# Optimization experiments

Hardware: AMD Instinct MI355X
Metric: run time of the kernel (lower is better)

Reference implementation:

```python
import jax, jax.numpy as jnp
import numpy as np

N, F, H = 22, 448, 64
LN_EPS = 1e-5


def _layernorm(h, g, b):
    mu = h.mean(axis=-1, keepdims=True)
    var = ((h - mu) ** 2).mean(axis=-1, keepdims=True)
    return (h - mu) / jnp.sqrt(var + LN_EPS) * g + b


def setup_inputs() -> dict:
    key = jax.random.key(0)
    ks = jax.random.split(key, 16)
    B = 128
    x = jax.random.normal(ks[0], (B, N, F), dtype=jnp.float32)
    s = lambda fan_in: 1.0 / np.sqrt(fan_in)
    # correlation-branch edge_weight_net: Linear(2F,64) -> ReLU -> Linear(64,1) -> Sigmoid
    cw1 = jax.random.uniform(ks[1], (2 * F, 64), jnp.float32, -s(2 * F), s(2 * F))
    cb1 = jax.random.uniform(ks[2], (64,), jnp.float32, -s(2 * F), s(2 * F))
    cw2 = jax.random.uniform(ks[3], (64, 1), jnp.float32, -s(64), s(64))
    cb2 = jax.random.uniform(ks[4], (1,), jnp.float32, -s(64), s(64))
    # semantic branch
    emb = jax.random.normal(ks[5], (N, H), dtype=jnp.float32) * 0.01
    D = 2 * H + 2 * F
    sw1 = jax.random.uniform(ks[6], (D, H), jnp.float32, -s(D), s(D))
    sb1 = jax.random.uniform(ks[7], (H,), jnp.float32, -s(D), s(D))
    ln_g = jnp.ones((H,), jnp.float32)
    ln_b = jnp.zeros((H,), jnp.float32)
    sw2 = jax.random.uniform(ks[8], (H, H // 2), jnp.float32, -s(H), s(H))
    sb2 = jax.random.uniform(ks[9], (H // 2,), jnp.float32, -s(H), s(H))
    sw3 = jax.random.uniform(ks[10], (H // 2, 1), jnp.float32, -s(H // 2), s(H // 2))
    sb3 = jax.random.uniform(ks[11], (1,), jnp.float32, -s(H // 2), s(H // 2))
    thr = jnp.asarray(0.3, jnp.float32)
    alpha_p = jnp.asarray(0.6, jnp.float32)
    return dict(x=x, cw1=cw1, cb1=cb1, cw2=cw2, cb2=cb2, emb=emb,
                sw1=sw1, sb1=sb1, ln_g=ln_g, ln_b=ln_b,
                sw2=sw2, sb2=sb2, sw3=sw3, sb3=sb3,
                thr=thr, alpha_p=alpha_p)


def reference(x, cw1, cb1, cw2, cb2, emb, sw1, sb1, ln_g, ln_b,
              sw2, sb2, sw3, sb3, thr, alpha_p):
    B, n, f = x.shape
    eye = jnp.eye(n, dtype=x.dtype)[None]

    # ---- Correlation graph ----
    xc = x - x.mean(axis=-1, keepdims=True)
    std = jnp.std(x, axis=-1, ddof=1, keepdims=True) + 1e-8  # torch std is unbiased
    xn = xc / std
    corr = jnp.abs(jnp.einsum('bif,bjf->bij', xn, xn) / f)
    # pairwise edge features (B,N,N,2F)
    xi = jnp.broadcast_to(x[:, :, None, :], (B, n, n, f))
    xj = jnp.broadcast_to(x[:, None, :, :], (B, n, n, f))
    ef = jnp.concatenate([xi, xj], axis=-1)
    h = jax.nn.relu(ef @ cw1 + cb1)
    w_corr = jax.nn.sigmoid((h @ cw2 + cb2)[..., 0])
    g_corr = corr * w_corr + eye

    # ---- Semantic graph ----
    ei = jnp.broadcast_to(emb[None, :, None, :], (B, n, n, H))
    ej = jnp.broadcast_to(emb[None, None, :, :], (B, n, n, H))
    sf = jnp.concatenate([ei, ej, xi, xj], axis=-1)  # (B,N,N,2H+2F)
    h1 = jax.nn.relu(_layernorm(sf @ sw1 + sb1, ln_g, ln_b))
    h2 = jax.nn.relu(h1 @ sw2 + sb2)
    w_sem = jax.nn.sigmoid((h2 @ sw3 + sb3)[..., 0])  # (B,N,N)
    # original loop fills only i<j and mirrors; diagonal stays 0
    upper = jnp.triu(w_sem, k=1)
    adj = upper + jnp.swapaxes(upper, 1, 2)
    t = jax.nn.sigmoid(thr)
    adj = jnp.where(adj > t, adj, jnp.zeros_like(adj))
    g_sem = adj + eye

    # ---- Learned fusion ----
    alpha = jax.nn.sigmoid(alpha_p)
    return alpha * g_corr + (1.0 - alpha) * g_sem
```

## Files before the change

kernel.cpp:

```cpp
#include <hip/hip_runtime.h>
#include <math.h>

namespace {
constexpr int kN = 22;
constexpr int kF = 448;
constexpr int kNP = kN * kN;
constexpr int kXStr = 452;
constexpr int kSm1 = kN * kXStr + 2 * kN;
constexpr int kAStr = 36;
constexpr int kBStr = 68;
constexpr int kPStr = 68;
}

__global__ __launch_bounds__(256) void hgc_k1(
    const float* __restrict__ x,
    const float* __restrict__ cw1, const float* __restrict__ cb1,
    const float* __restrict__ emb,
    const float* __restrict__ sw1, const float* __restrict__ sb1,
    float* __restrict__ C, float* __restrict__ g,
    int M, int Mtiles, int nGemm)
{
    __shared__ __align__(16) float sm[kSm1];
    const int tid = threadIdx.x;

    if ((int)blockIdx.x < nGemm) {
        float* As = sm;
        float* Bs = sm + 64 * kAStr;
        const int bm = blockIdx.x % Mtiles;
        const int bn = blockIdx.x / Mtiles;
        const int m0 = bm * 32;

        const float* Wsrc =
            (bn == 0) ? cw1 :
            (bn == 1) ? cw1 + 448 * 64 :
            (bn == 2) ? sw1 + 128 * 64 :
                        sw1 + 576 * 64;

        const int tm = tid & 15;
        const int tn = tid >> 4;
        float acc[2][4];
        #pragma unroll
        for (int i = 0; i < 2; ++i)
            #pragma unroll
            for (int j = 0; j < 4; ++j) acc[i][j] = 0.f;

        for (int k0 = 0; k0 < kF; k0 += 64) {
            #pragma unroll
            for (int pass = 0; pass < 2; ++pass) {
                const int idx = tid + pass * 256;
                const int row = idx >> 4, kq = idx & 15;
                const int m = m0 + row;
                float4 v = {0, 0, 0, 0};
                if (m < M) v = *(const float4*)&x[(size_t)m * kF + k0 + kq * 4];
                As[(kq * 4 + 0) * kAStr + row] = v.x;
                As[(kq * 4 + 1) * kAStr + row] = v.y;
                As[(kq * 4 + 2) * kAStr + row] = v.z;
                As[(kq * 4 + 3) * kAStr + row] = v.w;
            }
            #pragma unroll
            for (int pass = 0; pass < 4; ++pass) {
                const int idx = tid + pass * 256;
                const int k = idx >> 4, nq = idx & 15;
                const float4 v = *(const float4*)&Wsrc[(size_t)(k0 + k) * 64 + nq * 4];
                *(float4*)&Bs[k * kBStr + nq * 4] = v;
            }
            __syncthreads();
            #pragma unroll 8
            for (int k = 0; k < 64; ++k) {
                const float2 a2 = *(const float2*)&As[k * kAStr + tm * 2];
                const float4 b4 = *(const float4*)&Bs[k * kBStr + tn * 4];
                acc[0][0] = fmaf(a2.x, b4.x, acc[0][0]);
                acc[0][1] = fmaf(a2.x, b4.y, acc[0][1]);
                acc[0][2] = fmaf(a2.x, b4.z, acc[0][2]);
                acc[0][3] = fmaf(a2.x, b4.w, acc[0][3]);
                acc[1][0] = fmaf(a2.y, b4.x, acc[1][0]);
                acc[1][1] = fmaf(a2.y, b4.y, acc[1][1]);
                acc[1][2] = fmaf(a2.y, b4.z, acc[1][2]);
                acc[1][3] = fmaf(a2.y, b4.w, acc[1][3]);
            }
            __syncthreads();
        }

        if (bn >= 2) {
            const float* W2 = sw1 + (bn == 2 ? 0 : 64) * 64;
            #pragma unroll
            for (int pass = 0; pass < 2; ++pass) {
                const int idx = tid + pass * 256;
                const int row = idx >> 4, kq = idx & 15;
                const int r = (m0 + row) % kN;
                const float4 v = *(const float4*)&emb[(size_t)r * 64 + kq * 4];
                As[(kq * 4 + 0) * kAStr + row] = v.x;
                As[(kq * 4 + 1) * kAStr + row] = v.y;
                As[(kq * 4 + 2) * kAStr + row] = v.z;
                As[(kq * 4 + 3) * kAStr + row] = v.w;
            }
            #pragma unroll
            for (int pass = 0; pass < 4; ++pass) {
                const int idx = tid + pass * 256;
                const int k = idx >> 4, nq = idx & 15;
                const float4 v = *(const float4*)&W2[(size_t)k * 64 + nq * 4];
                *(float4*)&Bs[k * kBStr + nq * 4] = v;
            }
            __syncthreads();
            #pragma unroll 8
            for (int k = 0; k < 64; ++k) {
                const float2 a2 = *(const float2*)&As[k * kAStr + tm * 2];
                const float4 b4 = *(const float4*)&Bs[k * kBStr + tn * 4];
                acc[0][0] = fmaf(a2.x, b4.x, acc[0][0]);
                acc[0][1] = fmaf(a2.x, b4.y, acc[0][1]);
                acc[0][2] = fmaf(a2.x, b4.z, acc[0][2]);
                acc[0][3] = fmaf(a2.x, b4.w, acc[0][3]);
                acc[1][0] = fmaf(a2.y, b4.x, acc[1][0]);
                acc[1][1] = fmaf(a2.y, b4.y, acc[1][1]);
                acc[1][2] = fmaf(a2.y, b4.z, acc[1][2]);
                acc[1][3] = fmaf(a2.y, b4.w, acc[1][3]);
            }
        }

        float4 bias = {0, 0, 0, 0};
        if (bn == 0)      bias = *(const float4*)&cb1[tn * 4];
        else if (bn == 2) bias = *(const float4*)&sb1[tn * 4];
        #pragma unroll
        for (int i = 0; i < 2; ++i) {
            const int m = m0 + tm * 2 + i;
            if (m < M) {
                float4 o;
                o.x = acc[i][0] + bias.x; o.y = acc[i][1] + bias.y;
                o.z = acc[i][2] + bias.z; o.w = acc[i][3] + bias.w;
                *(float4*)&C[(size_t)m * 256 + bn * 64 + tn * 4] = o;
            }
        }
    } else {
        float* smu = sm + kN * kXStr;
        float* sis = smu + kN;
        const int cb = blockIdx.x - nGemm;
        const int b = cb >> 1;
        const int r0 = (cb & 1) * 11;

        const float4* xb4 = (const float4*)(x + (size_t)b * (kN * kF));
        for (int idx = tid; idx < kN * kF / 4; idx += 256) {
            const float4 v = xb4[idx];
            const int r = idx / 112;
            const int k = (idx - r * 112) * 4;
            float* d = sm + r * kXStr + k;
            d[0] = v.x; d[1] = v.y; d[2] = v.z; d[3] = v.w;
        }
        __syncthreads();

        {
            const int wid = tid >> 6, lane = tid & 63;
            for (int r = wid; r < kN; r += 4) {
                const float* row = sm + r * kXStr;
                float s = 0.f;
                #pragma unroll
                for (int c = 0; c < 7; ++c) s += row[c * 64 + lane];
                #pragma unroll
                for (int o = 32; o; o >>= 1) s += __shfl_xor(s, o, 64);
                const float mean = s * (1.f / 448.f);
                float ss = 0.f;
                #pragma unroll
                for (int c = 0; c < 7; ++c) { const float d = row[c * 64 + lane] - mean; ss = fmaf(d, d, ss); }
                #pragma unroll
                for (int o = 32; o; o >>= 1) ss += __shfl_xor(ss, o, 64);
                if (lane == 0) {
                    smu[r] = mean;
                    sis[r] = 1.f / (sqrtf(ss * (1.f / 447.f)) + 1e-8f);
                }
            }
        }
        __syncthreads();

        for (int p = tid; p < 11 * kN; p += 256) {
            const int pi = p / 22;
            const int i = r0 + pi, j = p - pi * 22;
            const float4* ri = (const float4*)(sm + i * kXStr);
            const float4* rj = (const float4*)(sm + j * kXStr);
            float dot = 0.f;
            for (int q = 0; q < 112; ++q) {
                const float4 a = ri[q], bq = rj[q];
                dot = fmaf(a.x, bq.x, dot); dot = fmaf(a.y, bq.y, dot);
                dot = fmaf(a.z, bq.z, dot); dot = fmaf(a.w, bq.w, dot);
            }
            const float c = (dot - 448.f * smu[i] * smu[j]) * sis[i] * sis[j] * (1.f / 448.f);
            g[(size_t)b * kNP + i * 22 + j] = fabsf(c);
        }
    }
}

__global__ __launch_bounds__(256) void hgc_k2(
    const float* __restrict__ C, const float* __restrict__ g,
    const float* __restrict__ cw2, const float* __restrict__ cb2,
    const float* __restrict__ sw2, const float* __restrict__ sb2,
    const float* __restrict__ sw3, const float* __restrict__ sb3,
    const float* __restrict__ ln_g, const float* __restrict__ ln_b,
    const float* __restrict__ thr, const float* __restrict__ alpha_p,
    float* __restrict__ out)
{
    __shared__ __align__(16) float sp[4 * kN * kPStr];
    __shared__ float sg[kNP];
    __shared__ __align__(16) float sw2s[2048];
    __shared__ float scw2[64], slng[64], slnb[64], ssw3[32], ssb2[32];
    __shared__ float vbuf[32 * 66];

    const int tid = threadIdx.x;
    const int b   = blockIdx.x >> 2;
    const int pb  = blockIdx.x & 3;

    #pragma unroll
    for (int a = 0; a < 4; ++a) {
        float* dst = sp + a * kN * kPStr;
        for (int idx = tid; idx < 352; idx += 256) {
            const int r = idx >> 4, kq = idx & 15;
            const float4 v = *(const float4*)&C[((size_t)(b * 22 + r)) * 256 + a * 64 + kq * 4];
            *(float4*)&dst[r * kPStr + kq * 4] = v;
        }
    }
    for (int idx = tid; idx < kNP; idx += 256) sg[idx] = g[(size_t)b * kNP + idx];
    {
        const float4* s4 = (const float4*)sw2;
        for (int idx = tid; idx < 512; idx += 256)
            *((float4*)(sw2s + idx * 4)) = s4[idx];
    }
    if (tid < 64)       { scw2[tid] = cw2[tid]; slng[tid] = ln_g[tid]; slnb[tid] = ln_b[tid]; }
    else if (tid < 96)  { ssw3[tid - 64] = sw3[tid - 64]; }
    else if (tid < 128) { ssb2[tid - 96] = sb2[tid - 96]; }
    __syncthreads();

    const int pl = tid >> 3;
    const int t  = tid & 7;
    const float* sa1 = sp;
    const float* sa2 = sp + kN * kPStr;
    const float* su1 = sp + 2 * kN * kPStr;
    const float* su2 = sp + 3 * kN * kPStr;

    for (int ch = 0; ch < 4; ++ch) {
        const int lp = ch * 32 + pl;
        const bool valid = lp < 121;
        const int p = valid ? (pb * 121 + lp) : 0;
        const int i = p / 22, j = p - (p / 22) * 22;

        float zc = 0.f;
        {
            const float* pa1 = sa1 + i * kPStr + t * 8;
            const float* pa2 = sa2 + j * kPStr + t * 8;
            #pragma unroll
            for (int c = 0; c < 8; ++c) {
                const float h = fmaxf(pa1[c] + pa2[c], 0.f);
                zc = fmaf(h, scw2[t * 8 + c], zc);
            }
            zc += __shfl_xor(zc, 1, 64); zc += __shfl_xor(zc, 2, 64); zc += __shfl_xor(zc, 4, 64);
        }
        const float wc = 1.f / (1.f + __expf(-(zc + cb2[0])));

        const int lo = (i < j) ? i : j, hi = (i < j) ? j : i;
        const float* pu1 = su1 + lo * kPStr + t * 8;
        const float* pu2 = su2 + hi * kPStr + t * 8;
        float raw[8];
        float s1 = 0.f;
        #pragma unroll
        for (int c = 0; c < 8; ++c) { raw[c] = pu1[c] + pu2[c]; s1 += raw[c]; }
        s1 += __shfl_xor(s1, 1, 64); s1 += __shfl_xor(s1, 2, 64); s1 += __shfl_xor(s1, 4, 64);
        const float mean = s1 * (1.f / 64.f);
        float s2 = 0.f;
        #pragma unroll
        for (int c = 0; c < 8; ++c) { const float d = raw[c] - mean; s2 = fmaf(d, d, s2); }
        s2 += __shfl_xor(s2, 1, 64); s2 += __shfl_xor(s2, 2, 64); s2 += __shfl_xor(s2, 4, 64);
        const float rstd = rsqrtf(s2 * (1.f / 64.f) + 1e-5f);
        {
            float* vb = vbuf + pl * 66 + t * 8;
            #pragma unroll
            for (int c = 0; c < 8; ++c) {
                const int k = t * 8 + c;
                float v = (raw[c] - mean) * rstd;
                v = fmaf(v, slng[k], slnb[k]);
                vb[c] = fmaxf(v, 0.f);
            }
        }
        __syncthreads();

        float4 acc = {0, 0, 0, 0};
        {
            const float* vb = vbuf + pl * 66;
            for (int k = 0; k < 64; ++k) {
                const float v = vb[k];
                const float4 w = *((const float4*)(sw2s + k * 32 + t * 4));
                acc.x = fmaf(v, w.x, acc.x); acc.y = fmaf(v, w.y, acc.y);
                acc.z = fmaf(v, w.z, acc.z); acc.w = fmaf(v, w.w, acc.w);
            }
        }
        float z2;
        {
            const int o0 = t * 4;
            z2  = fmaxf(acc.x + ssb2[o0 + 0], 0.f) * ssw3[o0 + 0];
            z2 += fmaxf(acc.y + ssb2[o0 + 1], 0.f) * ssw3[o0 + 1];
            z2 += fmaxf(acc.z + ssb2[o0 + 2], 0.f) * ssw3[o0 + 2];
            z2 += fmaxf(acc.w + ssb2[o0 + 3], 0.f) * ssw3[o0 + 3];
            z2 += __shfl_xor(z2, 1, 64); z2 += __shfl_xor(z2, 2, 64); z2 += __shfl_xor(z2, 4, 64);
        }

        if (valid && t == 0) {
            float gsem;
            if (i == j) {
                gsem = 1.f;
            } else {
                const float wsem = 1.f / (1.f + expf(-(z2 + sb3[0])));
                const float tt   = 1.f / (1.f + expf(-thr[0]));
                gsem = (wsem > tt) ? wsem : 0.f;
            }
            const float alpha = 1.f / (1.f + __expf(-alpha_p[0]));
            const float gcorr = fmaf(sg[p], wc, (i == j) ? 1.f : 0.f);
            out[(size_t)b * kNP + p] = fmaf(alpha, gcorr, (1.f - alpha) * gsem);
        }
    }
}

extern "C" void kernel_launch(void* const* d_in, const int* in_sizes, int n_in,
                              void* d_out, int out_size, void* d_ws, size_t ws_size,
                              hipStream_t stream)
{
    (void)n_in; (void)out_size; (void)ws_size;
    const float* x     = (const float*)d_in[0];
    const float* cw1   = (const float*)d_in[1];
    const float* cb1   = (const float*)d_in[2];
    const float* cw2   = (const float*)d_in[3];
    const float* cb2   = (const float*)d_in[4];
    const float* emb   = (const float*)d_in[5];
    const float* sw1   = (const float*)d_in[6];
    const float* sb1   = (const float*)d_in[7];
    const float* ln_g  = (const float*)d_in[8];
    const float* ln_b  = (const float*)d_in[9];
    const float* sw2   = (const float*)d_in[10];
    const float* sb2   = (const float*)d_in[11];
    const float* sw3   = (const float*)d_in[12];
    const float* sb3   = (const float*)d_in[13];
    const float* thr   = (const float*)d_in[14];
    const float* alpha = (const float*)d_in[15];
    float* out = (float*)d_out;
    float* ws  = (float*)d_ws;

    const int B = in_sizes[0] / (kN * kF);
    const int M = kN * B;
    const int Mtiles = (M + 31) / 32;
    const int nGemm = Mtiles * 4;

    float* C = ws;
    float* g = ws + (size_t)M * 256;

    hipLaunchKernelGGL(hgc_k1, dim3(nGemm + 2 * B), dim3(256), 0, stream,
                       x, cw1, cb1, emb, sw1, sb1, C, g, M, Mtiles, nGemm);
    hipLaunchKernelGGL(hgc_k2, dim3(4 * B), dim3(256), 0, stream,
                       C, g, cw2, cb2, sw2, sb2, sw3, sb3, ln_g, ln_b, thr, alpha, out);
}
```

Before: 125.2 us.

## Exploit correlation symmetry, merge per-batch blocks, drop block barrier in MLP loop

The correlation part of the first kernel now uses one block per batch instead of two. Each block computes only the upper-triangular pairs and mirrors each result, roughly halving the dot-product work, and the inner dot product uses four independent accumulators for more instruction-level parallelism. The second kernel processes two pair-chunks per batch instead of four, hoists scalar parameter loads and sigmoids out of the loop, and replaces the block-wide barrier with a wave-local LDS wait. That wait is only valid because each 8-thread group lives inside one wavefront. Fewer blocks in both kernels lowers launch and staging overhead, but the per-block serial work doubles and the GPU may be less evenly filled.

Measured after the change: 129.8 us. 1.04x slower.

```diff
diff --git a/kernel.cpp b/kernel.cpp
--- a/kernel.cpp
+++ b/kernel.cpp
@@ -133,9 +133,7 @@
     } else {
         float* smu = sm + kN * kXStr;
         float* sis = smu + kN;
-        const int cb = blockIdx.x - nGemm;
-        const int b = cb >> 1;
-        const int r0 = (cb & 1) * 11;
+        const int b = blockIdx.x - nGemm;
 
         const float4* xb4 = (const float4*)(x + (size_t)b * (kN * kF));
         for (int idx = tid; idx < kN * kF / 4; idx += 256) {
@@ -170,19 +168,23 @@
         }
         __syncthreads();
 
-        for (int p = tid; p < 11 * kN; p += 256) {
-            const int pi = p / 22;
-            const int i = r0 + pi, j = p - pi * 22;
+        if (tid < 253) {
+            int i = 0, rem = tid;
+            while (rem >= kN - i) { rem -= kN - i; ++i; }
+            const int j = i + rem;
             const float4* ri = (const float4*)(sm + i * kXStr);
             const float4* rj = (const float4*)(sm + j * kXStr);
-            float dot = 0.f;
+            float d0 = 0.f, d1 = 0.f, d2 = 0.f, d3 = 0.f;
             for (int q = 0; q < 112; ++q) {
                 const float4 a = ri[q], bq = rj[q];
-                dot = fmaf(a.x, bq.x, dot); dot = fmaf(a.y, bq.y, dot);
-                dot = fmaf(a.z, bq.z, dot); dot = fmaf(a.w, bq.w, dot);
-            }
+                d0 = fmaf(a.x, bq.x, d0); d1 = fmaf(a.y, bq.y, d1);
+                d2 = fmaf(a.z, bq.z, d2); d3 = fmaf(a.w, bq.w, d3);
+            }
+            const float dot = (d0 + d1) + (d2 + d3);
             const float c = (dot - 448.f * smu[i] * smu[j]) * sis[i] * sis[j] * (1.f / 448.f);
-            g[(size_t)b * kNP + i * 22 + j] = fabsf(c);
+            const float av = fabsf(c);
+            g[(size_t)b * kNP + i * 22 + j] = av;
+            if (i != j) g[(size_t)b * kNP + j * 22 + i] = av;
         }
     }
 }
@@ -203,8 +205,13 @@
     __shared__ float vbuf[32 * 66];
 
     const int tid = threadIdx.x;
-    const int b   = blockIdx.x >> 2;
-    const int pb  = blockIdx.x & 3;
+    const int b   = blockIdx.x >> 1;
+    const int pb  = blockIdx.x & 1;
+
+    const float cb2v  = cb2[0];
+    const float sb3v  = sb3[0];
+    const float tt    = 1.f / (1.f + expf(-thr[0]));
+    const float alpha = 1.f / (1.f + __expf(-alpha_p[0]));
 
     #pragma unroll
     for (int a = 0; a < 4; ++a) {
@@ -233,10 +240,10 @@
     const float* su1 = sp + 2 * kN * kPStr;
     const float* su2 = sp + 3 * kN * kPStr;
 
-    for (int ch = 0; ch < 4; ++ch) {
+    for (int ch = 0; ch < 8; ++ch) {
         const int lp = ch * 32 + pl;
-        const bool valid = lp < 121;
-        const int p = valid ? (pb * 121 + lp) : 0;
+        const bool valid = lp < 242;
+        const int p = valid ? (pb * 242 + lp) : 0;
         const int i = p / 22, j = p - (p / 22) * 22;
 
         float zc = 0.f;
@@ -250,7 +257,7 @@
             }
             zc += __shfl_xor(zc, 1, 64); zc += __shfl_xor(zc, 2, 64); zc += __shfl_xor(zc, 4, 64);
         }
-        const float wc = 1.f / (1.f + __expf(-(zc + cb2[0])));
+        const float wc = 1.f / (1.f + __expf(-(zc + cb2v)));
 
         const int lo = (i < j) ? i : j, hi = (i < j) ? j : i;
         const float* pu1 = su1 + lo * kPStr + t * 8;
@@ -276,7 +283,7 @@
                 vb[c] = fmaxf(v, 0.f);
             }
         }
-        __syncthreads();
+        asm volatile("s_waitcnt lgkmcnt(0)" ::: "memory");
 
         float4 acc = {0, 0, 0, 0};
         {
@@ -303,11 +310,9 @@
             if (i == j) {
                 gsem = 1.f;
             } else {
-                const float wsem = 1.f / (1.f + expf(-(z2 + sb3[0])));
-                const float tt   = 1.f / (1.f + expf(-thr[0]));
+                const float wsem = 1.f / (1.f + expf(-(z2 + sb3v)));
                 gsem = (wsem > tt) ? wsem : 0.f;
             }
-            const float alpha = 1.f / (1.f + __expf(-alpha_p[0]));
             const float gcorr = fmaf(sg[p], wc, (i == j) ? 1.f : 0.f);
             out[(size_t)b * kNP + p] = fmaf(alpha, gcorr, (1.f - alpha) * gsem);
         }
@@ -346,8 +351,8 @@
     float* C = ws;
     float* g = ws + (size_t)M * 256;
 
-    hipLaunchKernelGGL(hgc_k1, dim3(nGemm + 2 * B), dim3(256), 0, stream,
+    hipLaunchKernelGGL(hgc_k1, dim3(nGemm + B), dim3(256), 0, stream,
                        x, cw1, cb1, emb, sw1, sb1, C, g, M, Mtiles, nGemm);
-    hipLaunchKernelGGL(hgc_k2, dim3(4 * B), dim3(256), 0, stream,
+    hipLaunchKernelGGL(hgc_k2, dim3(2 * B), dim3(256), 0, stream,
                        C, g, cw2, cb2, sw2, sb2, sw3, sb3, ln_g, ln_b, thr, alpha, out);
 }
```
